# Performance work log

Hardware: AMD Instinct MI355X
Metric: run time of the kernel (lower is better)

Reference implementation:

```python
import jax, jax.numpy as jnp
import numpy as np

BATCH, IN, HID, OMID, OUT = 8192, 64, 1024, 128, 1
MAX_ITER = 8
EPS = 1e-3


def setup_inputs() -> dict:
    key = jax.random.key(0)
    ks = jax.random.split(key, 32)
    s_in, s_h = 1.0 / np.sqrt(IN), 1.0 / np.sqrt(HID)
    d = {"x": jax.random.normal(ks[0], (BATCH, IN), jnp.float32)}
    names = ["i", "f", "c", "o"]
    for j, n in enumerate(names):
        d[f"Wx{n}"] = jax.random.uniform(ks[1 + 4 * j], (HID, IN), jnp.float32, -s_in, s_in)
        d[f"bx{n}"] = jax.random.uniform(ks[2 + 4 * j], (HID,), jnp.float32, -s_in, s_in)
        d[f"Wh{n}"] = jax.random.uniform(ks[3 + 4 * j], (HID, HID), jnp.float32, -s_h, s_h)
        d[f"bh{n}"] = jax.random.uniform(ks[4 + 4 * j], (HID,), jnp.float32, -s_h, s_h)
    d["W_halt"] = jax.random.uniform(ks[20], (1, HID), jnp.float32, -s_h, s_h)
    d["b_halt"] = jax.random.uniform(ks[21], (1,), jnp.float32, -s_h, s_h)
    d["W1"] = jax.random.uniform(ks[22], (OMID, HID), jnp.float32, -s_h, s_h)
    d["b1"] = jax.random.uniform(ks[23], (OMID,), jnp.float32, -s_h, s_h)
    s_m = 1.0 / np.sqrt(OMID)
    d["W2"] = jax.random.uniform(ks[24], (OUT, OMID), jnp.float32, -s_m, s_m)
    d["b2"] = jax.random.uniform(ks[25], (OUT,), jnp.float32, -s_m, s_m)
    return d


def _act_forward(x, Wxi, bxi, Whi, bhi, Wxf, bxf, Whf, bhf, Wxc, bxc, Whc, bhc,
                 Wxo, bxo, Who, bho, W_halt, b_halt, W1, b1, W2, b2):
    B = x.shape[0]
    state0 = jnp.zeros((B, HID), x.dtype)
    cell0 = jnp.zeros((B, HID), x.dtype)
    p0 = jnp.zeros((B,), x.dtype)
    active0 = jnp.ones((B,), bool)

    def step(carry, t):
        state, cell, p_sum, active = carry
        # four LSTM-style gates (computed dense; masked update == torch's gather/scatter)
        i_g = jax.nn.sigmoid(x @ Wxi.T + bxi + state @ Whi.T + bhi)
        f_g = jax.nn.sigmoid(x @ Wxf.T + bxf + state @ Whf.T + bhf)
        c_g = jnp.tanh(x @ Wxc.T + bxc + state @ Whc.T + bhc)
        o_g = jax.nn.sigmoid(x @ Wxo.T + bxo + state @ Who.T + bho)
        am = active[:, None]
        cell = jnp.where(am, f_g * cell + i_g * c_g, cell)
        state = jnp.where(am, o_g * jnp.tanh(cell), state)
        out = jax.nn.sigmoid(jax.nn.relu(state @ W1.T + b1) @ W2.T + b2)  # (B, OUT)
        h = jax.nn.sigmoid(state @ W_halt.T + b_halt)[:, 0]               # (B,)
        p_new = p_sum + h
        last = t == MAX_ITER - 1
        finished = active & ((p_new >= 1.0 - EPS) | last)
        halt_rec = jnp.where(finished, 1.0 - p_sum, jnp.where(active, h, 0.0))
        p_sum = jnp.where(finished, 1.0, jnp.where(active, p_new, p_sum))
        out_rec = jnp.where(am, out, 0.0)
        active = active & ~finished
        return (state, cell, p_sum, active), (out_rec, halt_rec)

    _, (outs, halts) = jax.lax.scan(step, (state0, cell0, p0, active0), jnp.arange(MAX_ITER))
    # outs: (T, B, OUT), halts: (T, B); final = sum_t out_t * p_halt_t
    return jnp.einsum("tbo,tb->bo", outs, halts)


def reference(x, Wxi, bxi, Whi, bhi, Wxf, bxf, Whf, bhf, Wxc, bxc, Whc, bhc,
              Wxo, bxo, Who, bho, W_halt, b_halt, W1, b1, W2, b2):
    return _act_forward(x, Wxi, bxi, Whi, bhi, Wxf, bxf, Whf, bhf, Wxc, bxc, Whc, bhc,
                        Wxo, bxo, Who, bho, W_halt, b_halt, W1, b1, W2, b2)
```

## Files before the change

kernel.cpp:

```cpp
#include <hip/hip_runtime.h>
#include <hip/hip_bf16.h>

#define BATCH 8192
#define IN_DIM 64
#define HID 1024
#define KTOT 1088
#define NGATES 4096
#define OMID 128
#define NP 256
#define MAX_ITER 8

#define TM 128
#define TN 128
#define TK 64
#define TAILB 64

typedef __attribute__((ext_vector_type(8))) short short8;
typedef __attribute__((ext_vector_type(4))) float float4v;

__device__ __forceinline__ float bf2f(short s) {
    union { float f; unsigned u; } v; v.u = ((unsigned)(unsigned short)s) << 16; return v.f;
}
__device__ __forceinline__ short f2bf(float f) {
    union { float f; unsigned u; } v; v.f = f;
    unsigned r = v.u + 0x7fff + ((v.u >> 16) & 1);
    return (short)(r >> 16);
}
__device__ __forceinline__ float sigmoidf_(float x) {
    float xc = fminf(fmaxf(x, -30.f), 30.f);
    return 1.f / (1.f + __expf(-xc));
}
__device__ __forceinline__ float tanhf_(float x) {
    float xc = fminf(fmaxf(x, -15.f), 15.f);
    float e = __expf(2.f * xc);
    return (e - 1.f) / (e + 1.f);
}
__device__ __forceinline__ int aload(const int* p) {
    return __hip_atomic_load((int*)p, __ATOMIC_RELAXED, __HIP_MEMORY_SCOPE_AGENT);
}
__device__ __forceinline__ void astore(int* p, int v) {
    __hip_atomic_store(p, v, __ATOMIC_RELAXED, __HIP_MEMORY_SCOPE_AGENT);
}

__device__ __forceinline__ void gbar(int* bar, int phase, int tid) {
    __syncthreads();
    if (tid == 0) {
        __threadfence();
        __hip_atomic_fetch_add(bar, 1, __ATOMIC_ACQ_REL, __HIP_MEMORY_SCOPE_AGENT);
        while (aload(bar) < TAILB * phase)
            __builtin_amdgcn_s_sleep(8);
        __threadfence();
    }
    __syncthreads();
}

__device__ __forceinline__ void gates_tile(
    short* As, short* Bs, int tid,
    const short* __restrict__ A, const short* __restrict__ B,
    const float* __restrict__ bias_g, int K,
    float* __restrict__ cell, short* __restrict__ Aout,
    const int* __restrict__ ridx, int n_act, int m0, int bx)
{
    const int wave = tid >> 6, lane = tid & 63;
    const int wm = wave & 1, wn = wave >> 1;
    const int colq = lane & 15, q = lane >> 4;
    const int lrow8 = lane >> 3;
    const int lk    = (((lane & 7) ^ lrow8) * 8);
    const int n0 = bx * TN;

    int aoff[4][2], boff[4][2];
#pragma unroll
    for (int i = 0; i < 4; ++i) {
        const int Ra = wm * 64 + i * 16 + colq;
        const int Rb = wn * 64 + i * 16 + colq;
#pragma unroll
        for (int c2 = 0; c2 < 2; ++c2) {
            const int C = q + 4 * c2;
            aoff[i][c2] = Ra * TK + ((C ^ (Ra & 7)) << 3);
            boff[i][c2] = Rb * TK + ((C ^ (Rb & 7)) << 3);
        }
    }

    float4v acc[4][4];
#pragma unroll
    for (int i = 0; i < 4; ++i)
#pragma unroll
        for (int j = 0; j < 4; ++j) acc[i][j] = (float4v)0.f;

    const short* ga[4];
    const short* gb[4];
#pragma unroll
    for (int it = 0; it < 4; ++it) {
        const int rr = (wave * 4 + it) * 8;
        ga[it] = A + (size_t)ridx[m0 + rr + lrow8] * KTOT + lk;
        gb[it] = B + (size_t)(n0 + rr + lrow8) * KTOT + lk;
    }

    for (int k0 = 0; k0 < K; k0 += TK) {
#pragma unroll
        for (int it = 0; it < 4; ++it) {
            const int rr = (wave * 4 + it) * 8;
            __builtin_amdgcn_global_load_lds(
                (const __attribute__((address_space(1))) void*)ga[it],
                (__attribute__((address_space(3))) void*)(As + rr * TK), 16, 0, 0);
            __builtin_amdgcn_global_load_lds(
                (const __attribute__((address_space(1))) void*)gb[it],
                (__attribute__((address_space(3))) void*)(Bs + rr * TK), 16, 0, 0);
            ga[it] += TK; gb[it] += TK;
        }
        __syncthreads();
#pragma unroll
        for (int c2 = 0; c2 < 2; ++c2) {
            short8 af[4], bf[4];
#pragma unroll
            for (int i = 0; i < 4; ++i) {
                af[i] = *(const short8*)(As + aoff[i][c2]);
                bf[i] = *(const short8*)(Bs + boff[i][c2]);
            }
#pragma unroll
            for (int i = 0; i < 4; ++i)
#pragma unroll
                for (int j = 0; j < 4; ++j)
                    acc[i][j] = __builtin_amdgcn_mfma_f32_16x16x32_bf16(af[i], bf[j], acc[i][j], 0, 0, 0);
        }
        __syncthreads();
    }

    const int G = bx * 2 + wn;
    const int h = G * 16 + colq;
    const float bi  = bias_g[G * 64 +  0 + colq];
    const float bff = bias_g[G * 64 + 16 + colq];
    const float bc  = bias_g[G * 64 + 32 + colq];
    const float bo  = bias_g[G * 64 + 48 + colq];
#pragma unroll
    for (int i = 0; i < 4; ++i) {
        const int pbase = m0 + wm * 64 + i * 16 + q * 4;
#pragma unroll
        for (int r = 0; r < 4; ++r) {
            const int pos = pbase + r;
            if (pos < n_act) {
                const int row = ridx[pos];
                const float ig = sigmoidf_(acc[i][0][r] + bi);
                const float fg = sigmoidf_(acc[i][1][r] + bff);
                const float cg = tanhf_(acc[i][2][r] + bc);
                const float og = sigmoidf_(acc[i][3][r] + bo);
                const size_t ci = (size_t)row * HID + h;
                const float c = fg * cell[ci] + ig * cg;
                cell[ci] = c;
                Aout[(size_t)row * KTOT + h] = f2bf(og * tanhf_(c));
            }
        }
    }
    __syncthreads();
}

__device__ __forceinline__ void midfin_tile(
    short* As, short* Bs, int tid,
    const short* __restrict__ Anew, const short* __restrict__ P,
    const float* __restrict__ bias_p, const float* __restrict__ W_halt,
    const float* __restrict__ W2, const float* __restrict__ b2,
    float* __restrict__ outp, float* __restrict__ p_sum,
    const int* __restrict__ rprev, int* __restrict__ rnext,
    int* __restrict__ cnt, int t, int m0, int n_act)
{
    const int wave = tid >> 6, lane = tid & 63;
    const int wm = wave & 1, wn = wave >> 1;
    const int colq = lane & 15, q = lane >> 4;
    const int lrow8 = lane >> 3;
    const int lk    = (((lane & 7) ^ lrow8) * 8);

    float4v acc[4][4];
#pragma unroll
    for (int i = 0; i < 4; ++i)
#pragma unroll
        for (int j = 0; j < 4; ++j) acc[i][j] = (float4v)0.f;

    const short* ga[4];
    const short* gb[4];
#pragma unroll
    for (int it = 0; it < 4; ++it) {
        const int rr = (wave * 4 + it) * 8;
        ga[it] = Anew + (size_t)rprev[m0 + rr + lrow8] * KTOT + lk;
        gb[it] = P + (size_t)(rr + lrow8) * HID + lk;
    }
    int aoff[4][2], boff[4][2];
#pragma unroll
    for (int i = 0; i < 4; ++i) {
        const int Ra = wm * 64 + i * 16 + colq;
        const int Rb = wn * 64 + i * 16 + colq;
#pragma unroll
        for (int c2 = 0; c2 < 2; ++c2) {
            const int C = q + 4 * c2;
            aoff[i][c2] = Ra * TK + ((C ^ (Ra & 7)) << 3);
            boff[i][c2] = Rb * TK + ((C ^ (Rb & 7)) << 3);
        }
    }

    for (int k0 = 0; k0 < HID; k0 += TK) {
#pragma unroll
        for (int it = 0; it < 4; ++it) {
            const int rr = (wave * 4 + it) * 8;
            __builtin_amdgcn_global_load_lds(
                (const __attribute__((address_space(1))) void*)ga[it],
                (__attribute__((address_space(3))) void*)(As + rr * TK), 16, 0, 0);
            __builtin_amdgcn_global_load_lds(
                (const __attribute__((address_space(1))) void*)gb[it],
                (__attribute__((address_space(3))) void*)(Bs + rr * TK), 16, 0, 0);
            ga[it] += TK; gb[it] += TK;
        }
        __syncthreads();
#pragma unroll
        for (int c2 = 0; c2 < 2; ++c2) {
            short8 af[4], bf[4];
#pragma unroll
            for (int i = 0; i < 4; ++i) {
                af[i] = *(const short8*)(As + aoff[i][c2]);
                bf[i] = *(const short8*)(Bs + boff[i][c2]);
            }
#pragma unroll
            for (int i = 0; i < 4; ++i)
#pragma unroll
                for (int j = 0; j < 4; ++j)
                    acc[i][j] = __builtin_amdgcn_mfma_f32_16x16x32_bf16(af[i], bf[j], acc[i][j], 0, 0, 0);
        }
        __syncthreads();
    }

    float* red  = (float*)As;
    float* hbuf = ((float*)As) + 256;

    for (int s = 0; s < 32; ++s) {
        const int lr = wave * 32 + s;
        const int row = rprev[m0 + lr];
        const short* Ar = Anew + (size_t)row * KTOT + lane * 16;
        const short8 v0 = *(const short8*)Ar;
        const short8 v1 = *(const short8*)(Ar + 8);
        const float* Wh = W_halt + lane * 16;
        float hv = 0.f;
#pragma unroll
        for (int e = 0; e < 8; ++e) hv += bf2f(v0[e]) * Wh[e];
#pragma unroll
        for (int e = 0; e < 8; ++e) hv += bf2f(v1[e]) * Wh[8 + e];
#pragma unroll
        for (int o = 32; o > 0; o >>= 1) hv += __shfl_down(hv, o);
        if (lane == 0) hbuf[lr] = hv;
    }

    float pr[4][4];
#pragma unroll
    for (int i = 0; i < 4; ++i)
#pragma unroll
        for (int r = 0; r < 4; ++r) pr[i][r] = 0.f;
#pragma unroll
    for (int j = 0; j < 4; ++j) {
        const int col = wn * 64 + j * 16 + colq;
        const float b = bias_p[col];
        const float w2 = W2[col];
#pragma unroll
        for (int i = 0; i < 4; ++i)
#pragma unroll
            for (int r = 0; r < 4; ++r)
                pr[i][r] += fmaxf(acc[i][j][r] + b, 0.f) * w2;
    }
#pragma unroll
    for (int i = 0; i < 4; ++i)
#pragma unroll
        for (int r = 0; r < 4; ++r) {
            float v = pr[i][r];
            v += __shfl_down(v, 8, 16);
            v += __shfl_down(v, 4, 16);
            v += __shfl_down(v, 2, 16);
            v += __shfl_down(v, 1, 16);
            if (colq == 0)
                red[((((wn * 2) + wm) * 4 + i) * 4 + q) * 4 + r] = v;
        }
    __syncthreads();

    if (tid < TM) {
        const int pos = m0 + tid;
        if (pos < n_act) {
            const int lwm = tid >> 6, i = (tid >> 4) & 3, lq = (tid >> 2) & 3, r = tid & 3;
            const float odot = red[((lwm * 4 + i) * 4 + lq) * 4 + r]
                             + red[(((2 + lwm) * 4 + i) * 4 + lq) * 4 + r];
            const int row = rprev[pos];
            const float ov = sigmoidf_(odot + b2[0]);
            const float h  = sigmoidf_(hbuf[tid] + bias_p[OMID]);
            const float ps = p_sum[row];
            const float pn = ps + h;
            const bool fin = (pn >= 1.f - 1e-3f) || (t == MAX_ITER - 1);
            const float halt = fin ? (1.f - ps) : h;
            outp[row] += ov * halt;
            p_sum[row] = fin ? 1.f : pn;
            if (!fin) {
                const int d = atomicAdd(&cnt[t + 1], 1);
                astore(&rnext[d], row);
            }
        }
    }
    __syncthreads();
}

__global__ __launch_bounds__(256) void gates_k(
    const short* __restrict__ A, const short* __restrict__ B,
    const float* __restrict__ bias_g, int K,
    float* __restrict__ cell, short* __restrict__ Aout,
    const int* __restrict__ ridx, const int* __restrict__ cnt, int t)
{
    __shared__ short As[TM * TK];
    __shared__ short Bs[TN * TK];
    const int n_act = cnt[t];
    for (int by = blockIdx.y; by * TM < n_act; by += gridDim.y)
        gates_tile(As, Bs, threadIdx.x, A, B, bias_g, K, cell, Aout,
                   ridx, n_act, by * TM, blockIdx.x);
}

__global__ __launch_bounds__(256) void midfin_k(
    const short* __restrict__ Anew, const short* __restrict__ P,
    const float* __restrict__ bias_p, const float* __restrict__ W_halt,
    const float* __restrict__ W2, const float* __restrict__ b2,
    float* __restrict__ outp, float* __restrict__ p_sum,
    const int* __restrict__ rprev, int* __restrict__ rnext,
    int* __restrict__ cnt, int t)
{
    __shared__ short As[TM * TK];
    __shared__ short Bs[TN * TK];
    const int n_act = cnt[t];
    for (int tile = blockIdx.x; tile * TM < n_act; tile += gridDim.x)
        midfin_tile(As, Bs, threadIdx.x, Anew, P, bias_p, W_halt, W2, b2,
                    outp, p_sum, rprev, rnext, cnt, t, tile * TM, n_act);
}

__global__ __launch_bounds__(256) void tail_k(
    const short* __restrict__ Wg, const float* __restrict__ bias_g,
    const short* __restrict__ P, const float* __restrict__ bias_p,
    const float* __restrict__ W_halt, const float* __restrict__ W2,
    const float* __restrict__ b2,
    short* __restrict__ A0, short* __restrict__ A1,
    float* __restrict__ cell, float* __restrict__ outp,
    float* __restrict__ p_sum,
    int* __restrict__ ridx0, int* __restrict__ ridx1,
    int* __restrict__ cnt, int* __restrict__ bar)
{
    __shared__ short As[TM * TK];
    __shared__ short Bs[TN * TK];
    const int tid = threadIdx.x;
    int phase = 0;
    int t = 2;
    while (true) {
        short* Anew = (t & 1) ? A0 : A1;
        const int* rprev = (t & 1) ? ridx1 : ridx0;
        int* rnext = (t & 1) ? ridx0 : ridx1;
        const int n = aload(&cnt[t]);
        for (int tile = blockIdx.x; tile * TM < n; tile += gridDim.x)
            midfin_tile(As, Bs, tid, Anew, P, bias_p, W_halt, W2, b2,
                        outp, p_sum, rprev, rnext, cnt, t, tile * TM, n);
        if (t == MAX_ITER - 1) break;
        ++phase; gbar(bar, phase, tid);
        const int n1 = aload(&cnt[t + 1]);
        if (n1 == 0) break;
        {
            short* Aot = (t & 1) ? A1 : A0;
            const int ntiles = ((n1 + TM - 1) / TM) * (NGATES / TN);
            for (int e = blockIdx.x; e < ntiles; e += gridDim.x)
                gates_tile(As, Bs, tid, Anew, Wg, bias_g, KTOT, cell, Aot,
                           rnext, n1, (e >> 5) * TM, e & 31);
        }
        ++phase; gbar(bar, phase, tid);
        ++t;
    }
}

#define SETUP_INIT  (BATCH * KTOT)
#define SETUP_WG    (NGATES * KTOT)
#define SETUP_P     (NP * HID)
#define SETUP_TOT   (SETUP_INIT + SETUP_WG + SETUP_P)
__global__ __launch_bounds__(256) void setup_k(
    const float* __restrict__ x,
    const float* __restrict__ Whi, const float* __restrict__ Whf,
    const float* __restrict__ Whc, const float* __restrict__ Who,
    const float* __restrict__ Wxi, const float* __restrict__ Wxf,
    const float* __restrict__ Wxc, const float* __restrict__ Wxo,
    const float* __restrict__ bxi, const float* __restrict__ bhi,
    const float* __restrict__ bxf, const float* __restrict__ bhf,
    const float* __restrict__ bxc, const float* __restrict__ bhc,
    const float* __restrict__ bxo, const float* __restrict__ bho,
    const float* __restrict__ W1, const float* __restrict__ b1,
    const float* __restrict__ W_halt, const float* __restrict__ b_halt,
    short* __restrict__ A0, short* __restrict__ A1,
    float* __restrict__ cell, float* __restrict__ p_sum,
    int* __restrict__ ridx0, int* __restrict__ ridx1, int* __restrict__ cnt,
    int* __restrict__ bar, float* __restrict__ outp,
    short* __restrict__ Wg, float* __restrict__ bias_g,
    short* __restrict__ P, float* __restrict__ bias_p)
{
    int idx = blockIdx.x * 256 + threadIdx.x;
    if (idx < SETUP_INIT) {
        const int row = idx / KTOT, k = idx - row * KTOT;
        const short v = (k < HID) ? (short)0 : f2bf(x[row * IN_DIM + (k - HID)]);
        A0[idx] = v;
        A1[idx] = v;
        if (k < HID) cell[(size_t)row * HID + k] = 0.f;
        if (k == 0) {
            p_sum[row] = 0.f;
            outp[row] = 0.f;
            ridx0[row] = row;
            ridx1[row] = 0;
        }
        if (row == 0 && k <= MAX_ITER) cnt[k] = (k == 0) ? BATCH : 0;
        if (row == 1 && k == 0) bar[0] = 0;
        return;
    }
    idx -= SETUP_INIT;
    if (idx < SETUP_WG) {
        const int n = idx / KTOT, k = idx - n * KTOT;
        const int G = n >> 6, g = (n >> 4) & 3, q = n & 15;
        const int h = G * 16 + q;
        const float* Wh = (g == 0) ? Whi : (g == 1) ? Whf : (g == 2) ? Whc : Who;
        const float* Wx = (g == 0) ? Wxi : (g == 1) ? Wxf : (g == 2) ? Wxc : Wxo;
        const float v = (k < HID) ? Wh[h * HID + k] : Wx[h * IN_DIM + (k - HID)];
        Wg[idx] = f2bf(v);
        if (k == 0) {
            const float* bx = (g == 0) ? bxi : (g == 1) ? bxf : (g == 2) ? bxc : bxo;
            const float* bh = (g == 0) ? bhi : (g == 1) ? bhf : (g == 2) ? bhc : bho;
            bias_g[n] = bx[h] + bh[h];
        }
        return;
    }
    idx -= SETUP_WG;
    if (idx < SETUP_P) {
        const int n = idx >> 10, k = idx & 1023;
        const float v = (n < OMID) ? W1[n * HID + k] : (n == OMID ? W_halt[k] : 0.f);
        P[idx] = f2bf(v);
        if (k == 0) bias_p[n] = (n < OMID) ? b1[n] : (n == OMID ? b_halt[0] : 0.f);
    }
}

extern "C" void kernel_launch(void* const* d_in, const int* in_sizes, int n_in,
                              void* d_out, int out_size, void* d_ws, size_t ws_size,
                              hipStream_t stream) {
    const float* x    = (const float*)d_in[0];
    const float* Wxi  = (const float*)d_in[1];
    const float* bxi  = (const float*)d_in[2];
    const float* Whi  = (const float*)d_in[3];
    const float* bhi  = (const float*)d_in[4];
    const float* Wxf  = (const float*)d_in[5];
    const float* bxf  = (const float*)d_in[6];
    const float* Whf  = (const float*)d_in[7];
    const float* bhf  = (const float*)d_in[8];
    const float* Wxc  = (const float*)d_in[9];
    const float* bxc  = (const float*)d_in[10];
    const float* Whc  = (const float*)d_in[11];
    const float* bhc  = (const float*)d_in[12];
    const float* Wxo  = (const float*)d_in[13];
    const float* bxo  = (const float*)d_in[14];
    const float* Who  = (const float*)d_in[15];
    const float* bho  = (const float*)d_in[16];
    const float* W_halt = (const float*)d_in[17];
    const float* b_halt = (const float*)d_in[18];
    const float* W1   = (const float*)d_in[19];
    const float* b1   = (const float*)d_in[20];
    const float* W2   = (const float*)d_in[21];
    const float* b2   = (const float*)d_in[22];

    char* p = (char*)d_ws;
    auto carve = [&](size_t bytes) { char* r = p; p += (bytes + 255) & ~(size_t)255; return r; };
    short* A0     = (short*)carve((size_t)BATCH * KTOT * 2);
    short* A1     = (short*)carve((size_t)BATCH * KTOT * 2);
    short* Wg     = (short*)carve((size_t)NGATES * KTOT * 2);
    float* bias_g = (float*)carve((size_t)NGATES * 4);
    short* P      = (short*)carve((size_t)NP * HID * 2);
    float* bias_p = (float*)carve((size_t)NP * 4);
    float* cell   = (float*)carve((size_t)BATCH * HID * 4);
    float* p_sum  = (float*)carve((size_t)BATCH * 4);
    int*   ridx0  = (int*)carve((size_t)BATCH * 4);
    int*   ridx1  = (int*)carve((size_t)BATCH * 4);
    int*   cnt    = (int*)carve((size_t)(MAX_ITER + 1) * 4);
    int*   bar    = (int*)carve(256);
    float* outp   = (float*)d_out;

    setup_k<<<(SETUP_TOT + 255) / 256, 256, 0, stream>>>(
        x, Whi, Whf, Whc, Who, Wxi, Wxf, Wxc, Wxo,
        bxi, bhi, bxf, bhf, bxc, bhc, bxo, bho,
        W1, b1, W_halt, b_halt,
        A0, A1, cell, p_sum, ridx0, ridx1, cnt, bar, outp,
        Wg, bias_g, P, bias_p);

    gates_k<<<dim3(NGATES / TN, 32), 256, 0, stream>>>(
        A0 + HID, Wg + HID, bias_g, IN_DIM, cell, A1, ridx0, cnt, 0);
    midfin_k<<<64, 256, 0, stream>>>(
        A1, P, bias_p, W_halt, W2, b2, outp, p_sum, ridx0, ridx1, cnt, 0);
    gates_k<<<dim3(NGATES / TN, 32), 256, 0, stream>>>(
        A1, Wg, bias_g, KTOT, cell, A0, ridx1, cnt, 1);
    midfin_k<<<64, 256, 0, stream>>>(
        A0, P, bias_p, W_halt, W2, b2, outp, p_sum, ridx1, ridx0, cnt, 1);
    gates_k<<<dim3(NGATES / TN, 16), 256, 0, stream>>>(
        A0, Wg, bias_g, KTOT, cell, A1, ridx0, cnt, 2);
    tail_k<<<TAILB, 256, 0, stream>>>(
        Wg, bias_g, P, bias_p, W_halt, W2, b2,
        A0, A1, cell, outp, p_sum, ridx0, ridx1, cnt, bar);
}
```

Before: 497.0 us.

## Fuse midfin stage into gates kernel using completion counter and consumer blocks

Removes the separate midfin kernel launches by having each gates_k block signal completion on an atomic counter. The first 64 blocks then spin until all blocks finish and run the output/halting stage in the same launch. The tail kernel is restructured so each iteration does gates then midfin, starting from t=3. This saves launch gaps but relies on all blocks being co-resident or making progress; the spinning consumer blocks could deadlock if not scheduled.

```diff
diff --git a/kernel.cpp b/kernel.cpp
--- a/kernel.cpp
+++ b/kernel.cpp
@@ -14,6 +14,7 @@
 #define TN 128
 #define TK 64
 #define TAILB 64
+#define NCONS 64
 
 typedef __attribute__((ext_vector_type(8))) short short8;
 typedef __attribute__((ext_vector_type(4))) float float4v;
@@ -304,30 +305,40 @@
     const short* __restrict__ A, const short* __restrict__ B,
     const float* __restrict__ bias_g, int K,
     float* __restrict__ cell, short* __restrict__ Aout,
-    const int* __restrict__ ridx, const int* __restrict__ cnt, int t)
+    const int* __restrict__ ridx, int* __restrict__ cnt, int t,
+    const short* __restrict__ P, const float* __restrict__ bias_p,
+    const float* __restrict__ W_halt, const float* __restrict__ W2,
+    const float* __restrict__ b2,
+    float* __restrict__ outp, float* __restrict__ p_sum,
+    int* __restrict__ rnext, int* __restrict__ done, int total_blk)
 {
     __shared__ short As[TM * TK];
     __shared__ short Bs[TN * TK];
-    const int n_act = cnt[t];
+    const int tid = threadIdx.x;
+    const int bid = blockIdx.x + blockIdx.y * gridDim.x;
+    const int n_act = aload(&cnt[t]);
+
     for (int by = blockIdx.y; by * TM < n_act; by += gridDim.y)
-        gates_tile(As, Bs, threadIdx.x, A, B, bias_g, K, cell, Aout,
+        gates_tile(As, Bs, tid, A, B, bias_g, K, cell, Aout,
                    ridx, n_act, by * TM, blockIdx.x);
-}
-
-__global__ __launch_bounds__(256) void midfin_k(
-    const short* __restrict__ Anew, const short* __restrict__ P,
-    const float* __restrict__ bias_p, const float* __restrict__ W_halt,
-    const float* __restrict__ W2, const float* __restrict__ b2,
-    float* __restrict__ outp, float* __restrict__ p_sum,
-    const int* __restrict__ rprev, int* __restrict__ rnext,
-    int* __restrict__ cnt, int t)
-{
-    __shared__ short As[TM * TK];
-    __shared__ short Bs[TN * TK];
-    const int n_act = cnt[t];
-    for (int tile = blockIdx.x; tile * TM < n_act; tile += gridDim.x)
-        midfin_tile(As, Bs, threadIdx.x, Anew, P, bias_p, W_halt, W2, b2,
-                    outp, p_sum, rprev, rnext, cnt, t, tile * TM, n_act);
+
+    __syncthreads();
+    if (tid == 0) {
+        __threadfence();
+        __hip_atomic_fetch_add(done, 1, __ATOMIC_ACQ_REL, __HIP_MEMORY_SCOPE_AGENT);
+    }
+
+    if (bid < NCONS) {
+        if (tid == 0) {
+            while (aload(done) < total_blk)
+                __builtin_amdgcn_s_sleep(8);
+            __threadfence();
+        }
+        __syncthreads();
+        for (int tile = bid; tile * TM < n_act; tile += NCONS)
+            midfin_tile(As, Bs, tid, Aout, P, bias_p, W_halt, W2, b2,
+                        outp, p_sum, ridx, rnext, cnt, t, tile * TM, n_act);
+    }
 }
 
 __global__ __launch_bounds__(256) void tail_k(
@@ -345,28 +356,23 @@
     __shared__ short Bs[TN * TK];
     const int tid = threadIdx.x;
     int phase = 0;
-    int t = 2;
-    while (true) {
-        short* Anew = (t & 1) ? A0 : A1;
-        const int* rprev = (t & 1) ? ridx1 : ridx0;
-        int* rnext = (t & 1) ? ridx0 : ridx1;
+    for (int t = 3; t < MAX_ITER; ++t) {
         const int n = aload(&cnt[t]);
+        if (n == 0) return;
+        const short* Ain = (t & 1) ? A1 : A0;
+        short*       Aot = (t & 1) ? A0 : A1;
+        int* Lt = (t & 1) ? ridx1 : ridx0;
+        int* Ln = (t & 1) ? ridx0 : ridx1;
+        const int ntiles = ((n + TM - 1) / TM) * (NGATES / TN);
+        for (int e = blockIdx.x; e < ntiles; e += gridDim.x)
+            gates_tile(As, Bs, tid, Ain, Wg, bias_g, KTOT, cell, Aot,
+                       Lt, n, (e >> 5) * TM, e & 31);
+        ++phase; gbar(bar, phase, tid);
         for (int tile = blockIdx.x; tile * TM < n; tile += gridDim.x)
-            midfin_tile(As, Bs, tid, Anew, P, bias_p, W_halt, W2, b2,
-                        outp, p_sum, rprev, rnext, cnt, t, tile * TM, n);
+            midfin_tile(As, Bs, tid, Aot, P, bias_p, W_halt, W2, b2,
+                        outp, p_sum, Lt, Ln, cnt, t, tile * TM, n);
         if (t == MAX_ITER - 1) break;
         ++phase; gbar(bar, phase, tid);
-        const int n1 = aload(&cnt[t + 1]);
-        if (n1 == 0) break;
-        {
-            short* Aot = (t & 1) ? A1 : A0;
-            const int ntiles = ((n1 + TM - 1) / TM) * (NGATES / TN);
-            for (int e = blockIdx.x; e < ntiles; e += gridDim.x)
-                gates_tile(As, Bs, tid, Anew, Wg, bias_g, KTOT, cell, Aot,
-                           rnext, n1, (e >> 5) * TM, e & 31);
-        }
-        ++phase; gbar(bar, phase, tid);
-        ++t;
     }
 }
 
@@ -389,7 +395,7 @@
     short* __restrict__ A0, short* __restrict__ A1,
     float* __restrict__ cell, float* __restrict__ p_sum,
     int* __restrict__ ridx0, int* __restrict__ ridx1, int* __restrict__ cnt,
-    int* __restrict__ bar, float* __restrict__ outp,
+    int* __restrict__ bar, int* __restrict__ done, float* __restrict__ outp,
     short* __restrict__ Wg, float* __restrict__ bias_g,
     short* __restrict__ P, float* __restrict__ bias_p)
 {
@@ -408,6 +414,7 @@
         }
         if (row == 0 && k <= MAX_ITER) cnt[k] = (k == 0) ? BATCH : 0;
         if (row == 1 && k == 0) bar[0] = 0;
+        if (row == 1 && k > 0 && k <= MAX_ITER) done[k - 1] = 0;
         return;
     }
     idx -= SETUP_INIT;
@@ -476,25 +483,25 @@
     int*   ridx1  = (int*)carve((size_t)BATCH * 4);
     int*   cnt    = (int*)carve((size_t)(MAX_ITER + 1) * 4);
     int*   bar    = (int*)carve(256);
+    int*   done   = (int*)carve((size_t)MAX_ITER * 4);
     float* outp   = (float*)d_out;
 
     setup_k<<<(SETUP_TOT + 255) / 256, 256, 0, stream>>>(
         x, Whi, Whf, Whc, Who, Wxi, Wxf, Wxc, Wxo,
         bxi, bhi, bxf, bhf, bxc, bhc, bxo, bho,
         W1, b1, W_halt, b_halt,
-        A0, A1, cell, p_sum, ridx0, ridx1, cnt, bar, outp,
+        A0, A1, cell, p_sum, ridx0, ridx1, cnt, bar, done, outp,
         Wg, bias_g, P, bias_p);
 
     gates_k<<<dim3(NGATES / TN, 32), 256, 0, stream>>>(
-        A0 + HID, Wg + HID, bias_g, IN_DIM, cell, A1, ridx0, cnt, 0);
-    midfin_k<<<64, 256, 0, stream>>>(
-        A1, P, bias_p, W_halt, W2, b2, outp, p_sum, ridx0, ridx1, cnt, 0);
+        A0 + HID, Wg + HID, bias_g, IN_DIM, cell, A1, ridx0, cnt, 0,
+        P, bias_p, W_halt, W2, b2, outp, p_sum, ridx1, &done[0], 32 * 32);
     gates_k<<<dim3(NGATES / TN, 32), 256, 0, stream>>>(
-        A1, Wg, bias_g, KTOT, cell, A0, ridx1, cnt, 1);
-    midfin_k<<<64, 256, 0, stream>>>(
-        A0, P, bias_p, W_halt, W2, b2, outp, p_sum, ridx1, ridx0, cnt, 1);
+        A1, Wg, bias_g, KTOT, cell, A0, ridx1, cnt, 1,
+        P, bias_p, W_halt, W2, b2, outp, p_sum, ridx0, &done[1], 32 * 32);
     gates_k<<<dim3(NGATES / TN, 16), 256, 0, stream>>>(
-        A0, Wg, bias_g, KTOT, cell, A1, ridx0, cnt, 2);
+        A0, Wg, bias_g, KTOT, cell, A1, ridx0, cnt, 2,
+        P, bias_p, W_halt, W2, b2, outp, p_sum, ridx1, &done[2], 32 * 16);
     tail_k<<<TAILB, 256, 0, stream>>>(
         Wg, bias_g, P, bias_p, W_halt, W2, b2,
         A0, A1, cell, outp, p_sum, ridx0, ridx1, cnt, bar);
```

Measured after the change: 928.5 us. +86.8%, slower.
